# Optimization experiments

Hardware: AMD Instinct MI355X
Metric: run time of the kernel (lower is better)

The kernel has to match this reference:

```python
import jax, jax.numpy as jnp
import numpy as np

B, T, D, H, L, INNER = 2, 2048, 1024, 16, 8, 4096
EPS = 1e-5
MASK_BIAS = -10000.0

def setup_inputs() -> dict:
    key = jax.random.key(0)
    ks = jax.random.split(key, 6)
    std = 0.02
    w = lambda k, shape: jax.random.normal(k, shape, jnp.float32) * std
    return {
        "inputs_embeds": jax.random.normal(ks[0], (B, T, D), jnp.float32),
        "attention_mask": jnp.ones((B, T), jnp.float32),
        "ln1_w": jnp.ones((L, D), jnp.float32), "ln1_b": jnp.zeros((L, D), jnp.float32),
        "attn_w": w(ks[1], (L, D, 3 * D)), "attn_b": jnp.zeros((L, 3 * D), jnp.float32),
        "proj_w": w(ks[2], (L, D, D)), "proj_b": jnp.zeros((L, D), jnp.float32),
        "ln2_w": jnp.ones((L, D), jnp.float32), "ln2_b": jnp.zeros((L, D), jnp.float32),
        "fc_w": w(ks[3], (L, D, INNER)), "fc_b": jnp.zeros((L, INNER), jnp.float32),
        "fcp_w": w(ks[4], (L, INNER, D)), "fcp_b": jnp.zeros((L, D), jnp.float32),
        "lnf_w": jnp.ones((D,), jnp.float32), "lnf_b": jnp.zeros((D,), jnp.float32),
    }

def _ln(x, w, b):
    m = jnp.mean(x, axis=-1, keepdims=True)
    v = jnp.var(x, axis=-1, keepdims=True)
    return (x - m) * jax.lax.rsqrt(v + EPS) * w + b

def reference(inputs_embeds, attention_mask, ln1_w, ln1_b, attn_w, attn_b,
              proj_w, proj_b, ln2_w, ln2_b, fc_w, fc_b, fcp_w, fcp_b,
              lnf_w, lnf_b):
    hd = D // H
    scale = 1.0 / np.sqrt(hd).astype(np.float32)
    causal = jnp.tril(jnp.ones((T, T), bool))            # [T,T]
    add_mask = (1.0 - attention_mask)[:, None, None, :] * MASK_BIAS  # [B,1,1,T]
    heads = lambda t: t.reshape(B, T, H, hd).transpose(0, 2, 1, 3)   # [B,H,T,hd]
    h = inputs_embeds  # dropout is identity at eval
    for i in range(L):
        # --- causal self-attention (manual QK^T / softmax / AV) ---
        x = _ln(h, ln1_w[i], ln1_b[i])
        qkv = x @ attn_w[i] + attn_b[i]                  # [B,T,3D]
        q, k, v = (heads(t) for t in jnp.split(qkv, 3, axis=-1))
        s = jnp.einsum('bhqd,bhkd->bhqk', q, k) * scale  # [B,H,T,T]
        s = jnp.where(causal, s, MASK_BIAS) + add_mask   # masked_fill then additive mask
        p = jax.nn.softmax(s, axis=-1)
        ctx = jnp.einsum('bhqk,bhkd->bhqd', p, v)
        ctx = ctx.transpose(0, 2, 1, 3).reshape(B, T, D)
        h = h + ctx @ proj_w[i] + proj_b[i]
        # --- feed-forward ---
        x = _ln(h, ln2_w[i], ln2_b[i])
        h = h + jax.nn.relu(x @ fc_w[i] + fc_b[i]) @ fcp_w[i] + fcp_b[i]
    return _ln(h, lnf_w, lnf_b)
```

## Files before the change

### kernel.cpp

```cpp
#include <hip/hip_runtime.h>
#include <math.h>

namespace {
constexpr int kB = 2;
constexpr int kT = 2048;
constexpr int kD = 1024;
constexpr int kH = 16;
constexpr int kL = 8;
constexpr int kInner = 4096;
constexpr int kM = kB * kT;
constexpr float kEps = 1e-5f;
}

typedef __attribute__((ext_vector_type(8))) short bf16x8;
typedef __attribute__((ext_vector_type(4))) float f32x4;
typedef __attribute__((ext_vector_type(16))) float f32x16;

typedef const __attribute__((address_space(1))) void* gas_t;
typedef __attribute__((address_space(3))) void* las_t;

__device__ __forceinline__ short f2bf(float f) {
  union { float f; unsigned u; } v{f};
  unsigned r = (v.u + 0x7FFF + ((v.u >> 16) & 1)) >> 16;
  return (short)r;
}

__device__ __forceinline__ unsigned cvtpk_bf16(float lo, float hi) {
  unsigned r;
  asm("v_cvt_pk_bf16_f32 %0, %1, %2" : "=v"(r) : "v"(lo), "v"(hi));
  return r;
}

__device__ __forceinline__ void half_swap(unsigned& a, unsigned& b, bool ishi) {
  const unsigned sel = ishi ? a : b;
  const unsigned got = (unsigned)__shfl_xor((int)sel, 32, 64);
  a = ishi ? got : a;
  b = ishi ? b : got;
}

template <typename OT>
__global__ __launch_bounds__(256) void ln_kernel(
    const float* __restrict__ in, const float* __restrict__ w,
    const float* __restrict__ b, OT* __restrict__ out) {
  const int row = blockIdx.x;
  const int tid = threadIdx.x;
  const float4 v = ((const float4*)(in + (size_t)row * kD))[tid];
  float sum = v.x + v.y + v.z + v.w;
  float sq = v.x * v.x + v.y * v.y + v.z * v.z + v.w * v.w;
#pragma unroll
  for (int off = 32; off > 0; off >>= 1) {
    sum += __shfl_down(sum, off);
    sq += __shfl_down(sq, off);
  }
  __shared__ float s1[4], s2[4];
  const int wave = tid >> 6, lane = tid & 63;
  if (lane == 0) { s1[wave] = sum; s2[wave] = sq; }
  __syncthreads();
  const float ts = s1[0] + s1[1] + s1[2] + s1[3];
  const float tq = s2[0] + s2[1] + s2[2] + s2[3];
  const float mean = ts * (1.0f / kD);
  const float var = tq * (1.0f / kD) - mean * mean;
  const float rs = rsqrtf(var + kEps);
  const float4 w4 = ((const float4*)w)[tid];
  const float4 b4 = ((const float4*)b)[tid];
  float4 o;
  o.x = (v.x - mean) * rs * w4.x + b4.x;
  o.y = (v.y - mean) * rs * w4.y + b4.y;
  o.z = (v.z - mean) * rs * w4.z + b4.z;
  o.w = (v.w - mean) * rs * w4.w + b4.w;
  if constexpr (sizeof(OT) == 4) {
    ((float4*)(out + (size_t)row * kD))[tid] = o;
  } else {
    short4 s4;
    s4.x = f2bf(o.x); s4.y = f2bf(o.y); s4.z = f2bf(o.z); s4.w = f2bf(o.w);
    ((short4*)(out + (size_t)row * kD))[tid] = s4;
  }
}

__global__ __launch_bounds__(256) void convT_kernel(
    const float* __restrict__ aw, const float* __restrict__ pw,
    const float* __restrict__ fw, const float* __restrict__ gw,
    short* __restrict__ awT, short* __restrict__ pwT,
    short* __restrict__ fwT, short* __restrict__ gwT) {
  __shared__ short t[64][66];
  int b = blockIdx.x;
  const float* src; short* dst; int K, N, tk, tn;
  if (b < 768)       { src = aw; dst = awT; K = 1024; N = 3072; tk = b / 48; tn = b % 48; }
  else if (b < 1024) { b -= 768;  src = pw; dst = pwT; K = 1024; N = 1024; tk = b / 16; tn = b % 16; }
  else if (b < 2048) { b -= 1024; src = fw; dst = fwT; K = 1024; N = 4096; tk = b / 64; tn = b % 64; }
  else               { b -= 2048; src = gw; dst = gwT; K = 4096; N = 1024; tk = b / 16; tn = b % 16; }
  const int k0 = tk * 64, n0 = tn * 64;
  const int tr = threadIdx.x >> 4, tc4 = (threadIdx.x & 15) << 2;
#pragma unroll
  for (int i = 0; i < 4; ++i) {
    const int k = tr + i * 16;
    const float4 v = *(const float4*)(src + (size_t)(k0 + k) * N + n0 + tc4);
    t[k][tc4 + 0] = f2bf(v.x); t[k][tc4 + 1] = f2bf(v.y);
    t[k][tc4 + 2] = f2bf(v.z); t[k][tc4 + 3] = f2bf(v.w);
  }
  __syncthreads();
#pragma unroll
  for (int i = 0; i < 4; ++i) {
    const int n = tr + i * 16;
    short4 o;
    o.x = t[tc4 + 0][n]; o.y = t[tc4 + 1][n];
    o.z = t[tc4 + 2][n]; o.w = t[tc4 + 3][n];
    *(short4*)(dst + (size_t)(n0 + n) * K + k0 + tc4) = o;
  }
}

template <int OUT, bool RELU>
__global__ __launch_bounds__(256) void mfma_gemm(
    const short* __restrict__ A, const short* __restrict__ BT,
    const float* __restrict__ bias, const float* __restrict__ res,
    void* __restrict__ Cout, int N, int K) {
  __shared__ __align__(16) short As[128 * 64];
  __shared__ __align__(16) short Bs[128 * 64];
  const int tid = threadIdx.x;
  const int w = tid >> 6, lane = tid & 63;
  const int n16 = lane & 15, quad = lane >> 4;
  const int m0 = blockIdx.y * 128, n0 = blockIdx.x * 128;
  const int wr = (w >> 1) * 64, wc = (w & 1) * 64;

  f32x4 acc[4][4];
#pragma unroll
  for (int i = 0; i < 4; ++i)
#pragma unroll
    for (int j = 0; j < 4; ++j) acc[i][j] = (f32x4)0.f;

  const int srow = lane >> 3;
  const int schunk = lane & 7;

  for (int k0 = 0; k0 < K; k0 += 64) {
#pragma unroll
    for (int s = 0; s < 4; ++s) {
      const int r = (w * 4 + s) * 8 + srow;
      const int cs = schunk ^ (r & 7);
      __builtin_amdgcn_global_load_lds(
          (gas_t)(const void*)(A + (size_t)(m0 + r) * K + k0 + cs * 8),
          (las_t)(void*)(As + (w * 4 + s) * 8 * 64), 16, 0, 0);
      __builtin_amdgcn_global_load_lds(
          (gas_t)(const void*)(BT + (size_t)(n0 + r) * K + k0 + cs * 8),
          (las_t)(void*)(Bs + (w * 4 + s) * 8 * 64), 16, 0, 0);
    }
    __syncthreads();
#pragma unroll
    for (int kc = 0; kc < 2; ++kc) {
      bf16x8 af[4], bfr[4];
#pragma unroll
      for (int i = 0; i < 4; ++i) {
        const int m = wr + i * 16 + n16;
        af[i] = *(const bf16x8*)(As + m * 64 + (((kc << 2) + quad) ^ (m & 7)) * 8);
        const int n = wc + i * 16 + n16;
        bfr[i] = *(const bf16x8*)(Bs + n * 64 + (((kc << 2) + quad) ^ (n & 7)) * 8);
      }
#pragma unroll
      for (int i = 0; i < 4; ++i)
#pragma unroll
        for (int j = 0; j < 4; ++j)
          acc[i][j] = __builtin_amdgcn_mfma_f32_16x16x32_bf16(af[i], bfr[j],
                                                              acc[i][j], 0, 0, 0);
    }
    __syncthreads();
  }

#pragma unroll
  for (int j = 0; j < 4; ++j) {
    const int n = n0 + wc + j * 16 + n16;
    const float bv = bias[n];
#pragma unroll
    for (int i = 0; i < 4; ++i) {
#pragma unroll
      for (int r = 0; r < 4; ++r) {
        const int m = m0 + wr + i * 16 + quad * 4 + r;
        float v = acc[i][j][r] + bv;
        if (OUT == 1) {
          ((float*)Cout)[(size_t)m * N + n] = v + res[(size_t)m * N + n];
        } else {
          if (RELU) v = fmaxf(v, 0.f);
          ((short*)Cout)[(size_t)m * N + n] = f2bf(v);
        }
      }
    }
  }
}

__global__ __launch_bounds__(256) void attn_kernel(
    const short* __restrict__ qkv, const float* __restrict__ amaskp,
    short* __restrict__ ctx) {
  __shared__ __align__(16) short smem[2][8192];

  const int tid = threadIdx.x;
  const int w = tid >> 6;
  const int lane = tid & 63;
  const int l31 = lane & 31;
  const int hi = lane >> 5;
  const int bh = blockIdx.x;
  const int bb = bh >> 4, hh = bh & 15;
  const int qb = gridDim.y - 1 - blockIdx.y;
  const int q0 = qb * 128;
  const int qw0 = q0 + w * 32;

  const short* base  = qkv + (size_t)bb * kT * 3072;
  const short* kbase = base + 1024 + hh * 64;
  const short* vbase = base + 2048 + hh * 64;
  const float* amp   = amaskp + bb * kT;

  bf16x8 qf[4];
  {
    const short* qp = base + (size_t)(qw0 + l31) * 3072 + hh * 64 + hi * 8;
#pragma unroll
    for (int mi = 0; mi < 4; ++mi) qf[mi] = *(const bf16x8*)(qp + mi * 16);
  }

  f32x16 O[2];
  O[0] = (f32x16)0.f;
  O[1] = (f32x16)0.f;
  float m_r = -1e30f, l_r = 0.f;

  const int krow = tid >> 3, kch = tid & 7;
  const int vk4 = tid >> 5, vd16 = (tid >> 3) & 3;
  const int vkin = (tid >> 1) & 3, vdh = tid & 1;
  const int wuni = (tid & 192) * 8;

  const unsigned vs0 = (unsigned)(size_t)(las_t)(void*)(&smem[0][4096]);
  const int g = lane >> 4;
  const unsigned vtr =
      vs0 + (unsigned)((g >> 1) * 1024 + (g & 1) * 128 + (lane & 15) * 8);

  auto STAGE = [&](int buf, int k0) {
    short* ks = &smem[buf][0];
    short* vs = &smem[buf][4096];
#pragma unroll
    for (int r2 = 0; r2 < 2; ++r2) {
      const int rr = r2 * 32 + krow;
      __builtin_amdgcn_global_load_lds(
          (gas_t)(const void*)(kbase + (size_t)(k0 + rr) * 3072 +
                               ((kch ^ (rr & 7)) << 3)),
          (las_t)(void*)(ks + r2 * 2048 + wuni), 16, 0, 0);
      const int key = k0 + r2 * 32 + vk4 * 4 + vkin;
      __builtin_amdgcn_global_load_lds(
          (gas_t)(const void*)(vbase + (size_t)key * 3072 + vd16 * 16 + vdh * 8),
          (las_t)(void*)(vs + r2 * 2048 + wuni), 16, 0, 0);
    }
  };

  const int kend = q0 + 128;
  STAGE(0, 0);
  __syncthreads();
  int cur = 0;

  for (int k0 = 0; k0 < kend; k0 += 64) {
    if (k0 + 64 < kend) STAGE(cur ^ 1, k0 + 64);

    if (k0 <= qw0 + 31) {
      const short* ks = &smem[cur][0];

      f32x16 st[2];
      st[0] = (f32x16)0.f;
      st[1] = (f32x16)0.f;
#pragma unroll
      for (int s = 0; s < 2; ++s) {
        const int row = s * 32 + l31;
        const short* kp = ks + row * 64;
#pragma unroll
        for (int mi = 0; mi < 4; ++mi) {
          const bf16x8 kf =
              *(const bf16x8*)(kp + (((2 * mi + hi) ^ (row & 7)) << 3));
          st[s] = __builtin_amdgcn_mfma_f32_32x32x16_bf16(kf, qf[mi], st[s],
                                                          0, 0, 0);
        }
      }

#pragma unroll
      for (int s = 0; s < 2; ++s) {
        const bool pm = (k0 + 32 * s + 31 > qw0);
#pragma unroll
        for (int rq = 0; rq < 4; ++rq) {
          const int kb_ = k0 + 32 * s + 8 * rq + 4 * hi;
          const float4 a4 = *(const float4*)(amp + kb_);
          const float amv0 = (1.f - a4.x) * -10000.f;
          const float amv1 = (1.f - a4.y) * -10000.f;
          const float amv2 = (1.f - a4.z) * -10000.f;
          const float amv3 = (1.f - a4.w) * -10000.f;
          float v0 = st[s][rq * 4 + 0] * 0.125f;
          float v1 = st[s][rq * 4 + 1] * 0.125f;
          float v2 = st[s][rq * 4 + 2] * 0.125f;
          float v3 = st[s][rq * 4 + 3] * 0.125f;
          if (pm) {
            const int q = qw0 + l31;
            if (kb_ + 0 > q) v0 = -10000.f;
            if (kb_ + 1 > q) v1 = -10000.f;
            if (kb_ + 2 > q) v2 = -10000.f;
            if (kb_ + 3 > q) v3 = -10000.f;
          }
          st[s][rq * 4 + 0] = v0 + amv0;
          st[s][rq * 4 + 1] = v1 + amv1;
          st[s][rq * 4 + 2] = v2 + amv2;
          st[s][rq * 4 + 3] = v3 + amv3;
        }
      }

      float mx = st[0][0];
#pragma unroll
      for (int r = 1; r < 16; ++r) mx = fmaxf(mx, st[0][r]);
#pragma unroll
      for (int r = 0; r < 16; ++r) mx = fmaxf(mx, st[1][r]);
      mx = fmaxf(mx, __shfl_xor(mx, 32, 64));
      const float mn = fmaxf(m_r, mx);
      const float al = __expf(m_r - mn);
      m_r = mn;
      float sum = 0.f;
#pragma unroll
      for (int s = 0; s < 2; ++s)
#pragma unroll
        for (int r = 0; r < 16; ++r) {
          const float p = __expf(st[s][r] - mn);
          st[s][r] = p;
          sum += p;
        }
      sum += __shfl_xor(sum, 32, 64);
      l_r = l_r * al + sum;
#pragma unroll
      for (int r = 0; r < 16; ++r) {
        O[0][r] *= al;
        O[1][r] *= al;
      }

      bf16x8 pf[4];
      const bool ishi = (hi != 0);
#pragma unroll
      for (int s = 0; s < 2; ++s) {
#pragma unroll
        for (int hf = 0; hf < 2; ++hf) {
          unsigned wa = cvtpk_bf16(st[s][8 * hf + 0], st[s][8 * hf + 1]);
          unsigned wc = cvtpk_bf16(st[s][8 * hf + 4], st[s][8 * hf + 5]);
          half_swap(wa, wc, ishi);
          unsigned wb = cvtpk_bf16(st[s][8 * hf + 2], st[s][8 * hf + 3]);
          unsigned wd = cvtpk_bf16(st[s][8 * hf + 6], st[s][8 * hf + 7]);
          half_swap(wb, wd, ishi);
          union { unsigned u[4]; bf16x8 h; } f;
          f.u[0] = wa; f.u[1] = wb; f.u[2] = wc; f.u[3] = wd;
          pf[s * 2 + hf] = f.h;
        }
      }

      unsigned long long tv[16];
      const unsigned vb_ = vtr + (unsigned)(cur << 14);
#pragma unroll
      for (int c = 0; c < 4; ++c)
#pragma unroll
        for (int di = 0; di < 2; ++di) {
          asm volatile("ds_read_b64_tr_b16 %0, %1 offset:%2"
                       : "=v"(tv[(c * 2 + di) * 2 + 0])
                       : "v"(vb_), "n"(c * 2048 + di * 256));
          asm volatile("ds_read_b64_tr_b16 %0, %1 offset:%2"
                       : "=v"(tv[(c * 2 + di) * 2 + 1])
                       : "v"(vb_), "n"(c * 2048 + di * 256 + 512));
        }
      asm volatile("s_waitcnt lgkmcnt(0)" ::: "memory");
      __builtin_amdgcn_sched_barrier(0);
#pragma unroll
      for (int c = 0; c < 4; ++c)
#pragma unroll
        for (int di = 0; di < 2; ++di) {
          union { unsigned long long q[2]; bf16x8 h; } vf_;
          vf_.q[0] = tv[(c * 2 + di) * 2 + 0];
          vf_.q[1] = tv[(c * 2 + di) * 2 + 1];
          O[di] = __builtin_amdgcn_mfma_f32_32x32x16_bf16(vf_.h, pf[c], O[di],
                                                          0, 0, 0);
        }
    }

    __syncthreads();
    cur ^= 1;
  }

  const float inv = 1.f / l_r;
  const size_t tok = (size_t)bb * kT + qw0 + l31;
  short* cp = ctx + tok * 1024 + hh * 64 + 4 * hi;
#pragma unroll
  for (int di = 0; di < 2; ++di)
#pragma unroll
    for (int rq = 0; rq < 4; ++rq) {
      short4 o4;
      o4.x = f2bf(O[di][rq * 4 + 0] * inv);
      o4.y = f2bf(O[di][rq * 4 + 1] * inv);
      o4.z = f2bf(O[di][rq * 4 + 2] * inv);
      o4.w = f2bf(O[di][rq * 4 + 3] * inv);
      *(short4*)(cp + di * 32 + rq * 8) = o4;
    }
}

extern "C" void kernel_launch(void* const* d_in, const int* in_sizes, int n_in,
                              void* d_out, int out_size, void* d_ws, size_t ws_size,
                              hipStream_t stream) {
  const float* emb   = (const float*)d_in[0];
  const float* amask = (const float*)d_in[1];
  const float* ln1w  = (const float*)d_in[2];
  const float* ln1b  = (const float*)d_in[3];
  const float* attnw = (const float*)d_in[4];
  const float* attnb = (const float*)d_in[5];
  const float* projw = (const float*)d_in[6];
  const float* projb = (const float*)d_in[7];
  const float* ln2w  = (const float*)d_in[8];
  const float* ln2b  = (const float*)d_in[9];
  const float* fcw   = (const float*)d_in[10];
  const float* fcb   = (const float*)d_in[11];
  const float* fcpw  = (const float*)d_in[12];
  const float* fcpb  = (const float*)d_in[13];
  const float* lnfw  = (const float*)d_in[14];
  const float* lnfb  = (const float*)d_in[15];
  float* out = (float*)d_out;

  float* h    = (float*)d_ws;
  short* xb   = (short*)(h + (size_t)kM * kD);
  short* ctxb = xb + (size_t)kM * kD;
  short* bigb = ctxb + (size_t)kM * kD;
  short* awT  = bigb + (size_t)kM * kInner;
  short* pwT  = awT + (size_t)3072 * 1024;
  short* fwT  = pwT + (size_t)1024 * 1024;
  short* gwT  = fwT + (size_t)4096 * 1024;

  hipMemcpyAsync(h, emb, sizeof(float) * (size_t)kM * kD,
                 hipMemcpyDeviceToDevice, stream);

  const dim3 blk(256);
  for (int l = 0; l < kL; ++l) {
    convT_kernel<<<3072, blk, 0, stream>>>(
        attnw + (size_t)l * kD * 3072, projw + (size_t)l * kD * kD,
        fcw + (size_t)l * kD * kInner, fcpw + (size_t)l * kInner * kD,
        awT, pwT, fwT, gwT);
    ln_kernel<short><<<kM, blk, 0, stream>>>(h, ln1w + l * kD, ln1b + l * kD, xb);
    mfma_gemm<0, false><<<dim3(3072 / 128, kM / 128), blk, 0, stream>>>(
        xb, awT, attnb + l * 3072, nullptr, bigb, 3072, 1024);
    attn_kernel<<<dim3(kB * kH, kT / 128), blk, 0, stream>>>(bigb, amask, ctxb);
    mfma_gemm<1, false><<<dim3(1024 / 128, kM / 128), blk, 0, stream>>>(
        ctxb, pwT, projb + l * kD, h, h, 1024, 1024);
    ln_kernel<short><<<kM, blk, 0, stream>>>(h, ln2w + l * kD, ln2b + l * kD, xb);
    mfma_gemm<0, true><<<dim3(4096 / 128, kM / 128), blk, 0, stream>>>(
        xb, fwT, fcb + l * kInner, nullptr, bigb, 4096, 1024);
    mfma_gemm<1, false><<<dim3(1024 / 128, kM / 128), blk, 0, stream>>>(
        bigb, gwT, fcpb + l * kD, h, h, 1024, 4096);
  }
  ln_kernel<float><<<kM, blk, 0, stream>>>(h, lnfw, lnfb, out);
}
```

Baseline: 2.514 ms.

## Enlarge GEMM tiles to 256xBN with 512 threads and double-buffered LDS

Replaces the 128x128 single-buffered GEMM with a templated kernel that uses 256-row tiles (256 or 128 columns) and 8 waves. Global-to-LDS loads are double-buffered so the next K-slice is fetched while the current one is computed. The kernel also adds an XCD-aware block-index swizzle and raises wave priority around the MFMA bursts. The aims are more operand reuse per tile, latency hiding, and better L2 locality. In exchange it uses more registers and LDS per block (up to 128 KB for BN=256), which could limit occupancy. The larger tiles also mean fewer blocks for the N=1024 GEMMs.

Result: slower. 2.580 ms (+2.6%).

```diff
diff --git a/kernel.cpp b/kernel.cpp
--- a/kernel.cpp
+++ b/kernel.cpp
@@ -109,67 +109,110 @@
   }
 }
 
-template <int OUT, bool RELU>
-__global__ __launch_bounds__(256) void mfma_gemm(
+template <int BN_, int OUT, bool RELU>
+__global__ __launch_bounds__(512, 2) void mfma_gemm2(
     const short* __restrict__ A, const short* __restrict__ BT,
     const float* __restrict__ bias, const float* __restrict__ res,
     void* __restrict__ Cout, int N, int K) {
-  __shared__ __align__(16) short As[128 * 64];
-  __shared__ __align__(16) short Bs[128 * 64];
+  constexpr int BM = 256;
+  constexpr int NJ = BN_ / 64;
+  constexpr int NJ2 = NJ / 2;
+  __shared__ __align__(16) short As[2][BM * 64];
+  __shared__ __align__(16) short Bs[2][BN_ * 64];
   const int tid = threadIdx.x;
   const int w = tid >> 6, lane = tid & 63;
   const int n16 = lane & 15, quad = lane >> 4;
-  const int m0 = blockIdx.y * 128, n0 = blockIdx.x * 128;
-  const int wr = (w >> 1) * 64, wc = (w & 1) * 64;
-
-  f32x4 acc[4][4];
-#pragma unroll
-  for (int i = 0; i < 4; ++i)
-#pragma unroll
-    for (int j = 0; j < 4; ++j) acc[i][j] = (f32x4)0.f;
-
-  const int srow = lane >> 3;
-  const int schunk = lane & 7;
+  const int gridN = N / BN_;
+  int bid = blockIdx.x;
+  const int nwg = gridDim.x;
+  if ((nwg & 7) == 0) bid = (bid & 7) * (nwg >> 3) + (bid >> 3);
+  const int m0 = (bid / gridN) * BM, n0 = (bid % gridN) * BN_;
+  const int wr = (w >> 2) * 128, wc = (w & 3) * (BN_ / 4);
+
+  const short* Ap = A + (size_t)m0 * K;
+  const short* Bp = BT + (size_t)n0 * K;
+
+  f32x4 acc[8][NJ];
+#pragma unroll
+  for (int i = 0; i < 8; ++i)
+#pragma unroll
+    for (int j = 0; j < NJ; ++j) acc[i][j] = (f32x4)0.f;
+
+  const int srow = tid >> 3;
+  const int schunk = tid & 7;
+
+  auto STAGE = [&](int buf, int k0) {
+#pragma unroll
+    for (int i = 0; i < 4; ++i) {
+      const int r = i * 64 + srow;
+      __builtin_amdgcn_global_load_lds(
+          (gas_t)(const void*)(Ap + (size_t)r * K + k0 + ((schunk ^ (r & 7)) << 3)),
+          (las_t)(void*)(As[buf] + (i * 64 + w * 8) * 64), 16, 0, 0);
+    }
+#pragma unroll
+    for (int i = 0; i < NJ; ++i) {
+      const int r = i * 64 + srow;
+      __builtin_amdgcn_global_load_lds(
+          (gas_t)(const void*)(Bp + (size_t)r * K + k0 + ((schunk ^ (r & 7)) << 3)),
+          (las_t)(void*)(Bs[buf] + (i * 64 + w * 8) * 64), 16, 0, 0);
+    }
+  };
+
+  STAGE(0, 0);
+  __syncthreads();
+  int cur = 0;
 
   for (int k0 = 0; k0 < K; k0 += 64) {
-#pragma unroll
-    for (int s = 0; s < 4; ++s) {
-      const int r = (w * 4 + s) * 8 + srow;
-      const int cs = schunk ^ (r & 7);
-      __builtin_amdgcn_global_load_lds(
-          (gas_t)(const void*)(A + (size_t)(m0 + r) * K + k0 + cs * 8),
-          (las_t)(void*)(As + (w * 4 + s) * 8 * 64), 16, 0, 0);
-      __builtin_amdgcn_global_load_lds(
-          (gas_t)(const void*)(BT + (size_t)(n0 + r) * K + k0 + cs * 8),
-          (las_t)(void*)(Bs + (w * 4 + s) * 8 * 64), 16, 0, 0);
+    if (k0 + 64 < K) STAGE(cur ^ 1, k0 + 64);
+    const short* as_ = As[cur];
+    const short* bs_ = Bs[cur];
+
+    bf16x8 bf[NJ][2];
+#pragma unroll
+    for (int j = 0; j < NJ; ++j) {
+      const int n = wc + j * 16 + n16;
+#pragma unroll
+      for (int kc = 0; kc < 2; ++kc)
+        bf[j][kc] =
+            *(const bf16x8*)(bs_ + n * 64 + ((((kc << 2) + quad) ^ (n & 7)) << 3));
+    }
+#pragma unroll
+    for (int qm = 0; qm < 2; ++qm) {
+      bf16x8 af[4][2];
+#pragma unroll
+      for (int i = 0; i < 4; ++i) {
+        const int m = wr + (qm * 4 + i) * 16 + n16;
+#pragma unroll
+        for (int kc = 0; kc < 2; ++kc)
+          af[i][kc] =
+              *(const bf16x8*)(as_ + m * 64 + ((((kc << 2) + quad) ^ (m & 7)) << 3));
+      }
+#pragma unroll
+      for (int qn = 0; qn < 2; ++qn) {
+        __builtin_amdgcn_s_setprio(1);
+#pragma unroll
+        for (int i = 0; i < 4; ++i)
+#pragma unroll
+          for (int j = 0; j < NJ2; ++j)
+#pragma unroll
+            for (int kc = 0; kc < 2; ++kc)
+              acc[qm * 4 + i][qn * NJ2 + j] =
+                  __builtin_amdgcn_mfma_f32_16x16x32_bf16(
+                      af[i][kc], bf[qn * NJ2 + j][kc],
+                      acc[qm * 4 + i][qn * NJ2 + j], 0, 0, 0);
+        __builtin_amdgcn_s_setprio(0);
+      }
     }
     __syncthreads();
-#pragma unroll
-    for (int kc = 0; kc < 2; ++kc) {
-      bf16x8 af[4], bfr[4];
-#pragma unroll
-      for (int i = 0; i < 4; ++i) {
-        const int m = wr + i * 16 + n16;
-        af[i] = *(const bf16x8*)(As + m * 64 + (((kc << 2) + quad) ^ (m & 7)) * 8);
-        const int n = wc + i * 16 + n16;
-        bfr[i] = *(const bf16x8*)(Bs + n * 64 + (((kc << 2) + quad) ^ (n & 7)) * 8);
-      }
-#pragma unroll
-      for (int i = 0; i < 4; ++i)
-#pragma unroll
-        for (int j = 0; j < 4; ++j)
-          acc[i][j] = __builtin_amdgcn_mfma_f32_16x16x32_bf16(af[i], bfr[j],
-                                                              acc[i][j], 0, 0, 0);
-    }
-    __syncthreads();
-  }
-
-#pragma unroll
-  for (int j = 0; j < 4; ++j) {
+    cur ^= 1;
+  }
+
+#pragma unroll
+  for (int j = 0; j < NJ; ++j) {
     const int n = n0 + wc + j * 16 + n16;
     const float bv = bias[n];
 #pragma unroll
-    for (int i = 0; i < 4; ++i) {
+    for (int i = 0; i < 8; ++i) {
 #pragma unroll
       for (int r = 0; r < 4; ++r) {
         const int m = m0 + wr + i * 16 + quad * 4 + r;
@@ -426,21 +469,22 @@
                  hipMemcpyDeviceToDevice, stream);
 
   const dim3 blk(256);
+  const dim3 blk512(512);
   for (int l = 0; l < kL; ++l) {
     convT_kernel<<<3072, blk, 0, stream>>>(
         attnw + (size_t)l * kD * 3072, projw + (size_t)l * kD * kD,
         fcw + (size_t)l * kD * kInner, fcpw + (size_t)l * kInner * kD,
         awT, pwT, fwT, gwT);
     ln_kernel<short><<<kM, blk, 0, stream>>>(h, ln1w + l * kD, ln1b + l * kD, xb);
-    mfma_gemm<0, false><<<dim3(3072 / 128, kM / 128), blk, 0, stream>>>(
+    mfma_gemm2<256, 0, false><<<(3072 / 256) * (kM / 256), blk512, 0, stream>>>(
         xb, awT, attnb + l * 3072, nullptr, bigb, 3072, 1024);
     attn_kernel<<<dim3(kB * kH, kT / 128), blk, 0, stream>>>(bigb, amask, ctxb);
-    mfma_gemm<1, false><<<dim3(1024 / 128, kM / 128), blk, 0, stream>>>(
+    mfma_gemm2<128, 1, false><<<(1024 / 128) * (kM / 256), blk512, 0, stream>>>(
         ctxb, pwT, projb + l * kD, h, h, 1024, 1024);
     ln_kernel<short><<<kM, blk, 0, stream>>>(h, ln2w + l * kD, ln2b + l * kD, xb);
-    mfma_gemm<0, true><<<dim3(4096 / 128, kM / 128), blk, 0, stream>>>(
+    mfma_gemm2<256, 0, true><<<(4096 / 256) * (kM / 256), blk512, 0, stream>>>(
         xb, fwT, fcb + l * kInner, nullptr, bigb, 4096, 1024);
-    mfma_gemm<1, false><<<dim3(1024 / 128, kM / 128), blk, 0, stream>>>(
+    mfma_gemm2<128, 1, false><<<(1024 / 128) * (kM / 256), blk512, 0, stream>>>(
         bigb, gwT, fcpb + l * kD, h, h, 1024, 4096);
   }
   ln_kernel<float><<<kM, blk, 0, stream>>>(h, lnfw, lnfb, out);
```

## Double-buffer GEMM LDS tiles with prefetch, XCD-aware block remap, MFMA priority

Applied to the files above, without the earlier changes.

Rewrites the bf16 MFMA GEMM to double-buffer the A/B tiles in LDS. The next K-slice is issued with global_load_lds while the current slice is being multiplied, and there is one barrier per iteration instead of two. The grid becomes 1D with a remap that spreads consecutive block IDs across 8 XCD groups, intended to improve L2 locality. It also raises wave priority around the MFMA block and sets launch_bounds to 2 blocks per CU. The cost is twice the LDS (64KB per block), which may limit occupancy, and heavier register use from holding both k-chunk fragments at once.

New measurement: 2.392 ms. 4.9% less time.

```diff
diff --git a/kernel.cpp b/kernel.cpp
--- a/kernel.cpp
+++ b/kernel.cpp
@@ -110,58 +110,82 @@
 }
 
 template <int OUT, bool RELU>
-__global__ __launch_bounds__(256) void mfma_gemm(
+__global__ __launch_bounds__(256, 2) void mfma_gemm3(
     const short* __restrict__ A, const short* __restrict__ BT,
     const float* __restrict__ bias, const float* __restrict__ res,
     void* __restrict__ Cout, int N, int K) {
-  __shared__ __align__(16) short As[128 * 64];
-  __shared__ __align__(16) short Bs[128 * 64];
+  __shared__ __align__(16) short As[2][128 * 64];
+  __shared__ __align__(16) short Bs[2][128 * 64];
   const int tid = threadIdx.x;
   const int w = tid >> 6, lane = tid & 63;
   const int n16 = lane & 15, quad = lane >> 4;
-  const int m0 = blockIdx.y * 128, n0 = blockIdx.x * 128;
+  const int gridN = N >> 7;
+  int bid = blockIdx.x;
+  const int nwg = gridDim.x;
+  bid = (bid & 7) * (nwg >> 3) + (bid >> 3);
+  const int m0 = (bid / gridN) * 128, n0 = (bid % gridN) * 128;
   const int wr = (w >> 1) * 64, wc = (w & 1) * 64;
 
+  const short* Ap = A + (size_t)m0 * K;
+  const short* Bp = BT + (size_t)n0 * K;
+
   f32x4 acc[4][4];
 #pragma unroll
   for (int i = 0; i < 4; ++i)
 #pragma unroll
     for (int j = 0; j < 4; ++j) acc[i][j] = (f32x4)0.f;
 
-  const int srow = lane >> 3;
-  const int schunk = lane & 7;
+  const int srow = tid >> 3;
+  const int schunk = tid & 7;
+
+  auto STAGE = [&](int buf, int k0) {
+#pragma unroll
+    for (int i = 0; i < 4; ++i) {
+      const int r = i * 32 + srow;
+      const int cs = (schunk ^ (r & 7)) << 3;
+      __builtin_amdgcn_global_load_lds(
+          (gas_t)(const void*)(Ap + (size_t)r * K + k0 + cs),
+          (las_t)(void*)(As[buf] + (i * 32 + w * 8) * 64), 16, 0, 0);
+      __builtin_amdgcn_global_load_lds(
+          (gas_t)(const void*)(Bp + (size_t)r * K + k0 + cs),
+          (las_t)(void*)(Bs[buf] + (i * 32 + w * 8) * 64), 16, 0, 0);
+    }
+  };
+
+  STAGE(0, 0);
+  __syncthreads();
+  int cur = 0;
 
   for (int k0 = 0; k0 < K; k0 += 64) {
-#pragma unroll
-    for (int s = 0; s < 4; ++s) {
-      const int r = (w * 4 + s) * 8 + srow;
-      const int cs = schunk ^ (r & 7);
-      __builtin_amdgcn_global_load_lds(
-          (gas_t)(const void*)(A + (size_t)(m0 + r) * K + k0 + cs * 8),
-          (las_t)(void*)(As + (w * 4 + s) * 8 * 64), 16, 0, 0);
-      __builtin_amdgcn_global_load_lds(
-          (gas_t)(const void*)(BT + (size_t)(n0 + r) * K + k0 + cs * 8),
-          (las_t)(void*)(Bs + (w * 4 + s) * 8 * 64), 16, 0, 0);
-    }
+    if (k0 + 64 < K) STAGE(cur ^ 1, k0 + 64);
+    const short* as_ = As[cur];
+    const short* bs_ = Bs[cur];
+
+    bf16x8 af[4][2], bf[4][2];
+#pragma unroll
+    for (int i = 0; i < 4; ++i) {
+      const int m = wr + i * 16 + n16;
+      const int n = wc + i * 16 + n16;
+#pragma unroll
+      for (int kc = 0; kc < 2; ++kc) {
+        af[i][kc] =
+            *(const bf16x8*)(as_ + m * 64 + ((((kc << 2) + quad) ^ (m & 7)) << 3));
+        bf[i][kc] =
+            *(const bf16x8*)(bs_ + n * 64 + ((((kc << 2) + quad) ^ (n & 7)) << 3));
+      }
+    }
+    __builtin_amdgcn_s_setprio(1);
+#pragma unroll
+    for (int i = 0; i < 4; ++i)
+#pragma unroll
+      for (int j = 0; j < 4; ++j)
+#pragma unroll
+        for (int kc = 0; kc < 2; ++kc)
+          acc[i][j] = __builtin_amdgcn_mfma_f32_16x16x32_bf16(af[i][kc], bf[j][kc],
+                                                              acc[i][j], 0, 0, 0);
+    __builtin_amdgcn_s_setprio(0);
     __syncthreads();
-#pragma unroll
-    for (int kc = 0; kc < 2; ++kc) {
-      bf16x8 af[4], bfr[4];
-#pragma unroll
-      for (int i = 0; i < 4; ++i) {
-        const int m = wr + i * 16 + n16;
-        af[i] = *(const bf16x8*)(As + m * 64 + (((kc << 2) + quad) ^ (m & 7)) * 8);
-        const int n = wc + i * 16 + n16;
-        bfr[i] = *(const bf16x8*)(Bs + n * 64 + (((kc << 2) + quad) ^ (n & 7)) * 8);
-      }
-#pragma unroll
-      for (int i = 0; i < 4; ++i)
-#pragma unroll
-        for (int j = 0; j < 4; ++j)
-          acc[i][j] = __builtin_amdgcn_mfma_f32_16x16x32_bf16(af[i], bfr[j],
-                                                              acc[i][j], 0, 0, 0);
-    }
-    __syncthreads();
+    cur ^= 1;
   }
 
 #pragma unroll
@@ -432,15 +456,15 @@
         fcw + (size_t)l * kD * kInner, fcpw + (size_t)l * kInner * kD,
         awT, pwT, fwT, gwT);
     ln_kernel<short><<<kM, blk, 0, stream>>>(h, ln1w + l * kD, ln1b + l * kD, xb);
-    mfma_gemm<0, false><<<dim3(3072 / 128, kM / 128), blk, 0, stream>>>(
+    mfma_gemm3<0, false><<<(3072 / 128) * (kM / 128), blk, 0, stream>>>(
         xb, awT, attnb + l * 3072, nullptr, bigb, 3072, 1024);
     attn_kernel<<<dim3(kB * kH, kT / 128), blk, 0, stream>>>(bigb, amask, ctxb);
-    mfma_gemm<1, false><<<dim3(1024 / 128, kM / 128), blk, 0, stream>>>(
+    mfma_gemm3<1, false><<<(1024 / 128) * (kM / 128), blk, 0, stream>>>(
         ctxb, pwT, projb + l * kD, h, h, 1024, 1024);
     ln_kernel<short><<<kM, blk, 0, stream>>>(h, ln2w + l * kD, ln2b + l * kD, xb);
-    mfma_gemm<0, true><<<dim3(4096 / 128, kM / 128), blk, 0, stream>>>(
+    mfma_gemm3<0, true><<<(4096 / 128) * (kM / 128), blk, 0, stream>>>(
         xb, fwT, fcb + l * kInner, nullptr, bigb, 4096, 1024);
-    mfma_gemm<1, false><<<dim3(1024 / 128, kM / 128), blk, 0, stream>>>(
+    mfma_gemm3<1, false><<<(1024 / 128) * (kM / 128), blk, 0, stream>>>(
         bigb, gwT, fcpb + l * kD, h, h, 1024, 4096);
   }
   ln_kernel<float><<<kM, blk, 0, stream>>>(h, lnfw, lnfb, out);
```
